# Kernel optimization log

Hardware: AMD Instinct MI355X
Metric: run time of the kernel (lower is better)

Reference implementation:

```python
import jax, jax.numpy as jnp
import numpy as np

EMBED = 1024
HEADS = 16
HEAD_DIM = EMBED // HEADS
BATCH = 2
SUM_LEN = 64
REG_LEN = 2048
BAR = REG_LEN // SUM_LEN  # regular tokens per bar
ROPE_BASE = 10000.0


def _rope_cos_sin(pos, dim):
    inv = 1.0 / (ROPE_BASE ** (jnp.arange(0, dim, 2, dtype=jnp.float32) / dim))
    f = pos[:, None].astype(jnp.float32) * inv[None, :]        # (L, dim/2)
    emb = jnp.concatenate([f, f], axis=-1)                     # (L, dim)
    return jnp.cos(emb)[None, None], jnp.sin(emb)[None, None]  # (1,1,L,dim)


def _rot_half(x):
    d = x.shape[-1] // 2
    return jnp.concatenate([-x[..., d:], x[..., :d]], axis=-1)


def _apply_rope(q, k, cos, sin):
    return q * cos + _rot_half(q) * sin, k * cos + _rot_half(k) * sin


def _linear(x, w, b):
    return x @ w + b  # w: (in, out) == torch W.T


def _split_heads(x):
    b, l, _ = x.shape
    return x.reshape(b, l, HEADS, HEAD_DIM).transpose(0, 2, 1, 3)  # (B,H,L,D)


def _merge_heads(x):
    b, h, l, d = x.shape
    return x.transpose(0, 2, 1, 3).reshape(b, l, h * d)


def _masked_attn(q, k, v, mask):
    # fp32 attention as in the torch autocast-disabled blocks
    qf, kf, vf = q.astype(jnp.float32), k.astype(jnp.float32), v.astype(jnp.float32)
    s = jnp.einsum('bhqd,bhkd->bhqk', qf, kf) / np.sqrt(HEAD_DIM).astype(np.float32)
    s = jnp.where(mask[None, None], s, -jnp.inf)  # every row has >=1 valid key
    p = jax.nn.softmax(s, axis=-1)
    return jnp.einsum('bhqk,bhkd->bhqd', p, vf)


def _build_masks():
    S, R = SUM_LEN, REG_LEN
    bar_of = np.arange(R) // BAR
    ss = np.tril(np.ones((S, S), dtype=bool))
    sr = bar_of[None, :] == np.arange(S)[:, None]
    summarize = np.concatenate([ss, sr], axis=1)              # (S, S+R)
    rs = np.arange(S)[None, :] <= bar_of[:, None]
    rr = (bar_of[None, :] == bar_of[:, None]) & (np.arange(R)[None, :] <= np.arange(R)[:, None])
    updating = np.concatenate([rs, rr], axis=1)               # (R, S+R)
    return jnp.asarray(summarize), jnp.asarray(updating)


def setup_inputs() -> dict:
    key = jax.random.key(0)
    ks = jax.random.split(key, 24)
    inp = {
        'sum_x': jax.random.normal(ks[0], (BATCH, SUM_LEN, EMBED), jnp.float32),
        'reg_x': jax.random.normal(ks[1], (BATCH, REG_LEN, EMBED), jnp.float32),
    }
    sm, um = _build_masks()
    inp['summarize_mask'] = sm
    inp['updating_mask'] = um
    names = ['wq_s', 'wk_s', 'wv_s', 'wo_s', 'wq_r', 'wk_r', 'wv_r', 'wo_r', 'wk2', 'wv2']
    for i, n in enumerate(names):
        inp[n] = jax.random.normal(ks[2 + i], (EMBED, EMBED), jnp.float32) * 0.02
        inp[n.replace('w', 'b', 1)] = jnp.zeros((EMBED,), jnp.float32)
    return inp


def reference(sum_x, reg_x, summarize_mask, updating_mask,
              wq_s, bq_s, wk_s, bk_s, wv_s, bv_s, wo_s, bo_s,
              wq_r, bq_r, wk_r, bk_r, wv_r, bv_r, wo_r, bo_r,
              wk2, bk2, wv2, bv2):
    B, S, E = sum_x.shape
    R = reg_x.shape[1]

    sum_q = _split_heads(_linear(sum_x, wq_s, bq_s))
    sum_k = _split_heads(_linear(sum_x, wk_s, bk_s))
    sum_v = _split_heads(_linear(sum_x, wv_s, bv_s))
    reg_q = _split_heads(_linear(reg_x, wq_r, bq_r))
    reg_k = _split_heads(_linear(reg_x, wk_r, bk_r))
    reg_v = _split_heads(_linear(reg_x, wv_r, bv_r))

    # RoPE: summaries at positions [0,S), regulars at positions [S, S+R)
    cos_s, sin_s = _rope_cos_sin(jnp.arange(S), HEAD_DIM)
    sum_q, sum_k = _apply_rope(sum_q, sum_k, cos_s, sin_s)
    cos_r, sin_r = _rope_cos_sin(jnp.arange(S, S + R), HEAD_DIM)
    reg_q, reg_k = _apply_rope(reg_q, reg_k, cos_r, sin_r)

    # Stage 1: summaries attend over [summary K/V ; regular K/V]
    k1 = jnp.concatenate([sum_k, reg_k], axis=2)
    v1 = jnp.concatenate([sum_v, reg_v], axis=2)
    sum_attn = _merge_heads(_masked_attn(sum_q, k1, v1, summarize_mask))  # (B,S,E)

    # Re-project summary output to K2/V2
    sum_k2 = _split_heads(_linear(sum_attn, wk2, bk2))
    sum_v2 = _split_heads(_linear(sum_attn, wv2, bv2))

    # Stage 2: regulars attend over [summary K2/V2 ; regular K/V]
    k2 = jnp.concatenate([sum_k2, reg_k], axis=2)
    v2 = jnp.concatenate([sum_v2, reg_v], axis=2)
    reg_attn = _merge_heads(_masked_attn(reg_q, k2, v2, updating_mask))   # (B,R,E)

    sum_output = _linear(sum_attn, wo_s, bo_s)
    reg_output = _linear(reg_attn, wo_r, bo_r)
    return sum_output, reg_output
```

## Files before the change

### kernel.cpp

```cpp
#include <hip/hip_runtime.h>
#include <stdint.h>

typedef unsigned short u16;
typedef unsigned int u32;
typedef __attribute__((ext_vector_type(8))) short short8;
typedef __attribute__((ext_vector_type(4))) float f32x4;

#define EMBED 1024
#define HEADS 16
#define HDIM 64
#define NBATCH 2
#define SLEN 64
#define RLEN 2048
#define TOTKV (SLEN + RLEN)

struct B10 { const float* p[10]; };
struct WSrc { const float* p[10]; };

__device__ __forceinline__ float bf2f(u16 u) {
  union { u32 i; float f; } v; v.i = ((u32)u) << 16; return v.f;
}
__device__ __forceinline__ u16 f2bf(float f) {
  union { float f; u32 i; } v; v.f = f;
  return (u16)((v.i + 0x7fffu + ((v.i >> 16) & 1u)) >> 16);
}
__device__ __forceinline__ void up2(u32 u, float& a, float& b) {
  union { u32 i; float f; } x, y;
  x.i = u << 16; y.i = u & 0xffff0000u;
  a = x.f; b = y.f;
}
__device__ __forceinline__ void gload16(const void* g, void* l) {
  __builtin_amdgcn_global_load_lds((const __attribute__((address_space(1))) u32*)g,
                                   (__attribute__((address_space(3))) u32*)l, 16, 0, 0);
}

__global__ __launch_bounds__(256)
void prepass_k(WSrc wsrc, u16* __restrict__ Wt,
               const float* __restrict__ sum_x, u16* __restrict__ sxb,
               const float* __restrict__ reg_x, u16* __restrict__ rxb,
               float* __restrict__ cosT, float* __restrict__ sinT)
{
  __shared__ float tile[64][65];
  int b = blockIdx.x, t = threadIdx.x;
  if (b < 2560) {
    int z = b >> 8, rem = b & 255;
    int n0 = (rem & 15) * 64, k0 = (rem >> 4) * 64;
    const float* src = wsrc.p[z];
    u16* out = Wt + (size_t)z * (EMBED * (size_t)EMBED);
    int r0 = t >> 4, c0 = (t & 15) * 4;
#pragma unroll
    for (int i = 0; i < 4; ++i) {
      int r = i * 16 + r0;
      float4 v = *(const float4*)(src + (size_t)(k0 + r) * EMBED + n0 + c0);
      tile[r][c0] = v.x; tile[r][c0 + 1] = v.y; tile[r][c0 + 2] = v.z; tile[r][c0 + 3] = v.w;
    }
    __syncthreads();
#pragma unroll
    for (int i = 0; i < 4; ++i) {
      int n = i * 16 + r0;
      uint2 o;
      o.x = (u32)f2bf(tile[c0][n]) | ((u32)f2bf(tile[c0 + 1][n]) << 16);
      o.y = (u32)f2bf(tile[c0 + 2][n]) | ((u32)f2bf(tile[c0 + 3][n]) << 16);
      *(uint2*)(out + (size_t)(n0 + n) * EMBED + k0 + c0) = o;
    }
  } else if (b < 6656) {
    int i = ((b - 2560) * 256 + t) * 4;
    if (i < (int)((size_t)NBATCH * RLEN * EMBED)) {
      float4 v = *(const float4*)(reg_x + i);
      uint2 o;
      o.x = (u32)f2bf(v.x) | ((u32)f2bf(v.y) << 16);
      o.y = (u32)f2bf(v.z) | ((u32)f2bf(v.w) << 16);
      *(uint2*)(rxb + i) = o;
    }
  } else if (b < 6784) {
    int i = ((b - 6656) * 256 + t) * 4;
    if (i < (int)((size_t)NBATCH * SLEN * EMBED)) {
      float4 v = *(const float4*)(sum_x + i);
      uint2 o;
      o.x = (u32)f2bf(v.x) | ((u32)f2bf(v.y) << 16);
      o.y = (u32)f2bf(v.z) | ((u32)f2bf(v.w) << 16);
      *(uint2*)(sxb + i) = o;
    }
  } else {
    int idx = (b - 6784) * 256 + t;
    if (idx < TOTKV * 32) {
      int pos = idx >> 5, i = idx & 31;
      float inv = powf(10000.0f, -(float)i / 32.0f);
      float a = (float)pos * inv;
      float s, c;
      sincosf(a, &s, &c);
      cosT[idx] = c; sinT[idx] = s;
    }
  }
}

__device__ __forceinline__ void gemm_core(const u16* __restrict__ A, const u16* __restrict__ Wt,
                                          int rowBase, int colBase, int lane, int w,
                                          u16* As, u16* Bs, f32x4 (&acc)[4][4]) {
  int wr = w >> 1, wc = w & 1;
  int lrow = lane >> 3;
  int lcol = ((lane & 7) ^ lrow) * 8;
  const u16* srcA = A + (size_t)(rowBase + w * 16 + lrow) * EMBED + lcol;
  const u16* srcB = Wt + (size_t)(colBase + w * 16 + lrow) * EMBED + lcol;
  u16* dA = As + w * 1024;
  u16* dB = Bs + w * 1024;
  int l15 = lane & 15, lg = lane >> 4;
  int aoff = l15 * 64 + ((lg ^ (l15 & 7)) * 8);
  const u16* fA = As + wr * 4096 + aoff;
  const u16* fB = Bs + wc * 4096 + aoff;

  for (int k0 = 0; k0 < EMBED; k0 += 64) {
    gload16(srcA + k0, dA);
    gload16(srcA + 8 * EMBED + k0, dA + 512);
    gload16(srcA + 64 * EMBED + k0, dA + 4096);
    gload16(srcA + 72 * EMBED + k0, dA + 4608);
    gload16(srcB + k0, dB);
    gload16(srcB + 8 * EMBED + k0, dB + 512);
    gload16(srcB + 64 * EMBED + k0, dB + 4096);
    gload16(srcB + 72 * EMBED + k0, dB + 4608);
    __syncthreads();
#pragma unroll
    for (int ks = 0; ks < 2; ++ks) {
      const u16* fAk = (const u16*)((uintptr_t)fA ^ (unsigned)(ks << 6));
      const u16* fBk = (const u16*)((uintptr_t)fB ^ (unsigned)(ks << 6));
      short8 af[4], bfv[4];
#pragma unroll
      for (int mi = 0; mi < 4; ++mi) af[mi] = *(const short8*)(fAk + mi * 1024);
#pragma unroll
      for (int ni = 0; ni < 4; ++ni) bfv[ni] = *(const short8*)(fBk + ni * 1024);
#pragma unroll
      for (int mi = 0; mi < 4; ++mi)
#pragma unroll
        for (int ni = 0; ni < 4; ++ni)
          acc[mi][ni] = __builtin_amdgcn_mfma_f32_16x16x32_bf16(af[mi], bfv[ni], acc[mi][ni], 0, 0, 0);
    }
    __syncthreads();
  }
}

__device__ __forceinline__ void gemm_epilogue(f32x4 (&acc)[4][4], int mode, void* outp,
                                              const float* bias, int rowBase, int colBase,
                                              int L, int posoff, int lane, int w,
                                              const float* cosT, const float* sinT) {
  int wr = w >> 1, wc = w & 1;
  int c15 = lane & 15, rgrp = (lane >> 4) * 4;
  if (mode == 2) {
    float* out = (float*)outp;
#pragma unroll
    for (int mi = 0; mi < 4; ++mi)
#pragma unroll
      for (int r = 0; r < 4; ++r) {
        int m = rowBase + wr * 64 + mi * 16 + rgrp + r;
#pragma unroll
        for (int ni = 0; ni < 4; ++ni) {
          int n = colBase + wc * 64 + ni * 16 + c15;
          out[(size_t)m * EMBED + n] = acc[mi][ni][r] + bias[n];
        }
      }
  } else {
    u16* out = (u16*)outp;
    int h = (colBase >> 6) + wc;
    bool dorope = (mode == 0);
#pragma unroll
    for (int mi = 0; mi < 4; ++mi)
#pragma unroll
      for (int r = 0; r < 4; ++r) {
        int m = rowBase + wr * 64 + mi * 16 + rgrp + r;
        int bidx = (m >= L) ? 1 : 0;
        int l = m - bidx * L;
        size_t obase = ((size_t)(bidx * HEADS + h) * L + l) * HDIM;
        if (dorope) {
          int pos = posoff + l;
#pragma unroll
          for (int ni = 0; ni < 2; ++ni) {
            int d = ni * 16 + c15;
            float c = cosT[pos * 32 + d], s = sinT[pos * 32 + d];
            float x0 = acc[mi][ni][r] + bias[h * 64 + d];
            float x2 = acc[mi][ni + 2][r] + bias[h * 64 + d + 32];
            out[obase + d]      = f2bf(x0 * c - x2 * s);
            out[obase + d + 32] = f2bf(x2 * c + x0 * s);
          }
        } else {
#pragma unroll
          for (int ni = 0; ni < 4; ++ni) {
            int d = ni * 16 + c15;
            out[obase + d] = f2bf(acc[mi][ni][r] + bias[h * 64 + d]);
          }
        }
      }
  }
}

__global__ __launch_bounds__(256)
void qkv_gemm_k(const u16* __restrict__ rxb, const u16* __restrict__ sxb,
                const u16* __restrict__ Wt_all, B10 biases,
                u16* Qs, u16* Ks, u16* Vs, u16* Qr, u16* Kr, u16* Vr,
                const float* __restrict__ cosT, const float* __restrict__ sinT)
{
  __shared__ __align__(128) u16 As[8192];
  __shared__ __align__(128) u16 Bs[8192];
  int bx = blockIdx.x, by = blockIdx.y, bz = blockIdx.z;

  bool issum = (by == 0);
  const u16* A = issum ? sxb : rxb;
  int rowBase = issum ? 0 : (by - 1) * 128;
  int L = issum ? SLEN : RLEN;
  int posoff = issum ? 0 : SLEN;
  int widx = issum ? bz : 4 + bz;
  const u16* Wt = Wt_all + (size_t)widx * EMBED * EMBED;
  const float* bias = biases.p[widx];
  u16* out = issum ? (bz == 0 ? Qs : (bz == 1 ? Ks : Vs))
                   : (bz == 0 ? Qr : (bz == 1 ? Kr : Vr));
  int mode = (bz < 2) ? 0 : 1;
  int colBase = bx * 128;
  int lane = threadIdx.x & 63, w = threadIdx.x >> 6;

  f32x4 acc[4][4] = {};
  gemm_core(A, Wt, rowBase, colBase, lane, w, As, Bs, acc);
  gemm_epilogue(acc, mode, out, bias, rowBase, colBase, L, posoff, lane, w, cosT, sinT);
}

__global__ __launch_bounds__(256)
void gemm_k(const u16* __restrict__ A,
            const u16* W0, const u16* W1, const u16* W2,
            const float* b0, const float* b1, const float* b2,
            void* o0, void* o1, void* o2,
            int L, int m0, int m1, int m2, int posoff,
            const float* __restrict__ cosT, const float* __restrict__ sinT)
{
  __shared__ __align__(128) u16 As[8192];
  __shared__ __align__(128) u16 Bs[8192];
  int bx = blockIdx.x, by = blockIdx.y, bz = blockIdx.z;
  const u16* Wt = (bz == 0) ? W0 : ((bz == 1) ? W1 : W2);
  const float* bias = (bz == 0) ? b0 : ((bz == 1) ? b1 : b2);
  void* outp = (bz == 0) ? o0 : ((bz == 1) ? o1 : o2);
  int mode = (bz == 0) ? m0 : ((bz == 1) ? m1 : m2);
  int rowBase = by * 128, colBase = bx * 128;
  int lane = threadIdx.x & 63, w = threadIdx.x >> 6;

  f32x4 acc[4][4] = {};
  gemm_core(A, Wt, rowBase, colBase, lane, w, As, Bs, acc);
  gemm_epilogue(acc, mode, outp, bias, rowBase, colBase, L, posoff, lane, w, cosT, sinT);
}

__global__ __launch_bounds__(256)
void gemm64_k(const u16* __restrict__ A, const u16* __restrict__ Wt,
              const float* __restrict__ bias, float* __restrict__ out)
{
  __shared__ __align__(128) u16 As[8192];
  __shared__ __align__(128) u16 Bs[4096];
  int rowBase = blockIdx.y * 128, colBase = blockIdx.x * 64;
  int lane = threadIdx.x & 63, w = threadIdx.x >> 6;
  int lrow = lane >> 3, lcol = ((lane & 7) ^ lrow) * 8;

  const u16* srcA = A + (size_t)(rowBase + w * 16 + lrow) * EMBED + lcol;
  const u16* srcB = Wt + (size_t)(colBase + w * 16 + lrow) * EMBED + lcol;
  u16* dA = As + w * 1024;
  u16* dB = Bs + w * 1024;
  int l15 = lane & 15, lg = lane >> 4;
  int aoff = l15 * 64 + ((lg ^ (l15 & 7)) * 8);
  const u16* fA = As + w * 2048 + aoff;
  const u16* fB = Bs + aoff;

  f32x4 acc[2][4] = {};
  for (int k0 = 0; k0 < EMBED; k0 += 64) {
    gload16(srcA + k0, dA);
    gload16(srcA + 8 * EMBED + k0, dA + 512);
    gload16(srcA + 64 * EMBED + k0, dA + 4096);
    gload16(srcA + 72 * EMBED + k0, dA + 4608);
    gload16(srcB + k0, dB);
    gload16(srcB + 8 * EMBED + k0, dB + 512);
    __syncthreads();
#pragma unroll
    for (int ks = 0; ks < 2; ++ks) {
      const u16* fAk = (const u16*)((uintptr_t)fA ^ (unsigned)(ks << 6));
      const u16* fBk = (const u16*)((uintptr_t)fB ^ (unsigned)(ks << 6));
      short8 af[2], bfv[4];
#pragma unroll
      for (int mi = 0; mi < 2; ++mi) af[mi] = *(const short8*)(fAk + mi * 1024);
#pragma unroll
      for (int ni = 0; ni < 4; ++ni) bfv[ni] = *(const short8*)(fBk + ni * 1024);
#pragma unroll
      for (int mi = 0; mi < 2; ++mi)
#pragma unroll
        for (int ni = 0; ni < 4; ++ni)
          acc[mi][ni] = __builtin_amdgcn_mfma_f32_16x16x32_bf16(af[mi], bfv[ni], acc[mi][ni], 0, 0, 0);
    }
    __syncthreads();
  }

  int c15 = lane & 15, rgrp = (lane >> 4) * 4;
#pragma unroll
  for (int mi = 0; mi < 2; ++mi)
#pragma unroll
    for (int r = 0; r < 4; ++r) {
      int m = rowBase + w * 32 + mi * 16 + rgrp + r;
#pragma unroll
      for (int ni = 0; ni < 4; ++ni) {
        int n = colBase + ni * 16 + c15;
        out[(size_t)m * EMBED + n] = acc[mi][ni][r] + bias[n];
      }
    }
}

__device__ __forceinline__ void loadq(const u16* qrow, float* qf) {
  const uint4* qp = (const uint4*)qrow;
#pragma unroll
  for (int c = 0; c < 8; ++c) {
    uint4 u = qp[c];
    up2(u.x, qf[c * 8 + 0], qf[c * 8 + 1]);
    up2(u.y, qf[c * 8 + 2], qf[c * 8 + 3]);
    up2(u.z, qf[c * 8 + 4], qf[c * 8 + 5]);
    up2(u.w, qf[c * 8 + 6], qf[c * 8 + 7]);
  }
}
__device__ __forceinline__ float dot64(const float* qf, const u16* krow) {
  const uint4* kp = (const uint4*)krow;
  float s = 0.f;
#pragma unroll
  for (int c = 0; c < 8; ++c) {
    uint4 u = kp[c];
    float a0, a1, a2, a3, a4, a5, a6, a7;
    up2(u.x, a0, a1); up2(u.y, a2, a3); up2(u.z, a4, a5); up2(u.w, a6, a7);
    s += qf[c * 8 + 0] * a0 + qf[c * 8 + 1] * a1 + qf[c * 8 + 2] * a2 + qf[c * 8 + 3] * a3
       + qf[c * 8 + 4] * a4 + qf[c * 8 + 5] * a5 + qf[c * 8 + 6] * a6 + qf[c * 8 + 7] * a7;
  }
  return s;
}

__global__ __launch_bounds__(256)
void attn1_k(const u16* __restrict__ Qs, const u16* __restrict__ Ks,
             const u16* __restrict__ Vs, const u16* __restrict__ Kr,
             const u16* __restrict__ Vr, u16* __restrict__ outA)
{
  int gw = blockIdx.x * 4 + (threadIdx.x >> 6);
  int bh = gw >> 6, qi = gw & 63;
  int b = bh >> 4, h = bh & 15;
  int lane = threadIdx.x & 63;
  const u16* qB = Qs + (size_t)bh * SLEN * HDIM;
  const u16* kS = Ks + (size_t)bh * SLEN * HDIM;
  const u16* vS = Vs + (size_t)bh * SLEN * HDIM;
  const u16* kR = Kr + (size_t)bh * RLEN * HDIM;
  const u16* vR = Vr + (size_t)bh * RLEN * HDIM;

  float qf[64];
  loadq(qB + qi * HDIM, qf);
  bool v1 = (lane <= qi);
  bool v2 = (lane < 32);
  float s1 = v1 ? dot64(qf, kS + lane * HDIM) : 0.f;
  float s2 = v2 ? dot64(qf, kR + (qi * 32 + lane) * HDIM) : 0.f;
  float sc1 = v1 ? s1 * 0.125f : -1e30f;
  float sc2 = v2 ? s2 * 0.125f : -1e30f;
  float mx = fmaxf(sc1, sc2);
#pragma unroll
  for (int off = 32; off; off >>= 1) mx = fmaxf(mx, __shfl_xor(mx, off));
  float e1 = v1 ? __expf(sc1 - mx) : 0.f;
  float e2 = v2 ? __expf(sc2 - mx) : 0.f;
  float sm = e1 + e2;
#pragma unroll
  for (int off = 32; off; off >>= 1) sm += __shfl_xor(sm, off);
  float inv = 1.f / sm;

  float a0 = 0.f, a1 = 0.f, a2 = 0.f, a3 = 0.f;
  const u16* vrow = vR + (size_t)qi * 32 * HDIM + lane;
#pragma unroll
  for (int j = 0; j < 64; j += 4) {
    a0 += __shfl(e1, j + 0) * bf2f(vS[(j + 0) * HDIM + lane]);
    a1 += __shfl(e1, j + 1) * bf2f(vS[(j + 1) * HDIM + lane]);
    a2 += __shfl(e1, j + 2) * bf2f(vS[(j + 2) * HDIM + lane]);
    a3 += __shfl(e1, j + 3) * bf2f(vS[(j + 3) * HDIM + lane]);
  }
#pragma unroll
  for (int j = 0; j < 32; j += 4) {
    a0 += __shfl(e2, j + 0) * bf2f(vrow[(j + 0) * HDIM]);
    a1 += __shfl(e2, j + 1) * bf2f(vrow[(j + 1) * HDIM]);
    a2 += __shfl(e2, j + 2) * bf2f(vrow[(j + 2) * HDIM]);
    a3 += __shfl(e2, j + 3) * bf2f(vrow[(j + 3) * HDIM]);
  }
  float accv = (a0 + a1) + (a2 + a3);
  outA[((size_t)(b * SLEN + qi)) * EMBED + h * HDIM + lane] = f2bf(accv * inv);
}

__global__ __launch_bounds__(256)
void attn2_k(const u16* __restrict__ Qr, const u16* __restrict__ Kr,
             const u16* __restrict__ Vr, const u16* __restrict__ Ks2,
             const u16* __restrict__ Vs2, u16* __restrict__ outA)
{
  __shared__ __align__(16) float Sf[32][104];
  __shared__ __align__(16) u16 Pb[32][104];
  __shared__ __align__(16) u16 Vt[64][104];

  int bar = blockIdx.x, bh = blockIdx.y;
  int b = bh >> 4, h = bh & 15;
  int nS = bar + 1;
  int tid = threadIdx.x, lane = tid & 63, w = tid >> 6;
  int l15 = lane & 15, lg = lane >> 4;

  const u16* qB = Qr + ((size_t)bh * RLEN + bar * 32) * HDIM;
  const u16* kS = Ks2 + (size_t)bh * SLEN * HDIM;
  const u16* kR = Kr + ((size_t)bh * RLEN + bar * 32) * HDIM;
  const u16* vS = Vs2 + (size_t)bh * SLEN * HDIM;
  const u16* vR = Vr + ((size_t)bh * RLEN + bar * 32) * HDIM;

  {
    int keyo = tid >> 3, dg = (tid & 7) * 8;
#pragma unroll
    for (int it = 0; it < 3; ++it) {
      int key = it * 32 + keyo;
      const u16* src = (key < 64) ? (vS + key * 64 + dg) : (vR + (key - 64) * 64 + dg);
      uint4 v = *(const uint4*)src;
#pragma unroll
      for (int wi = 0; wi < 4; ++wi) {
        u32 wv = (wi == 0) ? v.x : (wi == 1) ? v.y : (wi == 2) ? v.z : v.w;
        Vt[dg + 2 * wi][key]     = (u16)(wv & 0xffffu);
        Vt[dg + 2 * wi + 1][key] = (u16)(wv >> 16);
      }
    }
  }

#pragma unroll
  for (int i = 0; i < 3; ++i) {
    int t = w * 3 + i, r = t / 6, c = t % 6;
    const u16* arow = qB + (r * 16 + l15) * 64 + lg * 8;
    const u16* brow = (c < 4) ? (kS + (c * 16 + l15) * 64 + lg * 8)
                              : (kR + ((c - 4) * 16 + l15) * 64 + lg * 8);
    f32x4 acc = {};
    acc = __builtin_amdgcn_mfma_f32_16x16x32_bf16(*(const short8*)arow,
                                                  *(const short8*)brow, acc, 0, 0, 0);
    acc = __builtin_amdgcn_mfma_f32_16x16x32_bf16(*(const short8*)(arow + 32),
                                                  *(const short8*)(brow + 32), acc, 0, 0, 0);
#pragma unroll
    for (int j = 0; j < 4; ++j)
      Sf[r * 16 + lg * 4 + j][c * 16 + l15] = acc[j] * 0.125f;
  }
  __syncthreads();

  {
    int r = w * 8 + (lane >> 3), sub = lane & 7;
    float vals[12];
    float mx = -1e30f;
#pragma unroll
    for (int j = 0; j < 12; ++j) {
      int c = sub + 8 * j;
      bool valid = (c < nS) || (c >= 64 && c < 96 && (c - 64) <= r);
      float v = valid ? Sf[r][c] : -1e30f;
      vals[j] = v;
      mx = fmaxf(mx, v);
    }
#pragma unroll
    for (int off = 1; off < 8; off <<= 1) mx = fmaxf(mx, __shfl_xor(mx, off));
    float sm = 0.f;
#pragma unroll
    for (int j = 0; j < 12; ++j) {
      vals[j] = __expf(vals[j] - mx);
      sm += vals[j];
    }
#pragma unroll
    for (int off = 1; off < 8; off <<= 1) sm += __shfl_xor(sm, off);
    float inv = 1.f / sm;
#pragma unroll
    for (int j = 0; j < 12; ++j) {
      int c = sub + 8 * j;
      Pb[r][c] = f2bf(vals[j] * inv);
    }
  }
  __syncthreads();

#pragma unroll
  for (int i = 0; i < 2; ++i) {
    int t = w * 2 + i, r = t >> 2, dc = t & 3;
    f32x4 acc = {};
#pragma unroll
    for (int ks = 0; ks < 3; ++ks) {
      short8 a = *(const short8*)&Pb[r * 16 + l15][ks * 32 + lg * 8];
      short8 bb = *(const short8*)&Vt[dc * 16 + l15][ks * 32 + lg * 8];
      acc = __builtin_amdgcn_mfma_f32_16x16x32_bf16(a, bb, acc, 0, 0, 0);
    }
    int d = dc * 16 + l15;
#pragma unroll
    for (int j = 0; j < 4; ++j) {
      int qq = r * 16 + lg * 4 + j;
      int tt = bar * 32 + qq;
      outA[((size_t)(b * RLEN + tt)) * EMBED + h * 64 + d] = f2bf(acc[j]);
    }
  }
}

extern "C" void kernel_launch(void* const* d_in, const int* in_sizes, int n_in,
                              void* d_out, int out_size, void* d_ws, size_t ws_size,
                              hipStream_t stream) {
  const float* sum_x = (const float*)d_in[0];
  const float* reg_x = (const float*)d_in[1];
  const float* W[10]; const float* Bv[10];
  for (int i = 0; i < 10; ++i) {
    W[i] = (const float*)d_in[4 + 2 * i];
    Bv[i] = (const float*)d_in[5 + 2 * i];
  }

  char* ws = (char*)d_ws;
  size_t off = 0;
  auto alloc = [&](size_t bytes) -> void* {
    void* p = ws + off;
    off += (bytes + 255) & ~(size_t)255;
    return p;
  };

  const size_t SX = (size_t)NBATCH * SLEN * EMBED;
  const size_t RX = (size_t)NBATCH * RLEN * EMBED;

  float* cosT = (float*)alloc((size_t)TOTKV * 32 * 4);
  float* sinT = (float*)alloc((size_t)TOTKV * 32 * 4);
  u16* sxb = (u16*)alloc(SX * 2);
  u16* rxb = (u16*)alloc(RX * 2);
  u16* Wt  = (u16*)alloc((size_t)10 * EMBED * EMBED * 2);
  u16* Qs = (u16*)alloc(SX * 2);
  u16* Ks = (u16*)alloc(SX * 2);
  u16* Vs = (u16*)alloc(SX * 2);
  u16* Qr = (u16*)alloc(RX * 2);
  u16* Kr = (u16*)alloc(RX * 2);
  u16* Vr = (u16*)alloc(RX * 2);
  u16* sattn = (u16*)alloc(SX * 2);
  u16* Ks2 = (u16*)alloc(SX * 2);
  u16* Vs2 = (u16*)alloc(SX * 2);
  u16* rattn = (u16*)alloc(RX * 2);
  (void)ws_size; (void)in_sizes; (void)n_in; (void)out_size;

  WSrc wsrc;
  for (int i = 0; i < 10; ++i) wsrc.p[i] = W[i];
  B10 biases;
  for (int i = 0; i < 10; ++i) biases.p[i] = Bv[i];

  prepass_k<<<7048, 256, 0, stream>>>(wsrc, Wt, sum_x, sxb, reg_x, rxb, cosT, sinT);

#define WT(i) (Wt + (size_t)(i) * EMBED * EMBED)
  qkv_gemm_k<<<dim3(8, 33, 3), 256, 0, stream>>>(rxb, sxb, Wt, biases,
      Qs, Ks, Vs, Qr, Kr, Vr, cosT, sinT);
  attn1_k<<<512, 256, 0, stream>>>(Qs, Ks, Vs, Kr, Vr, sattn);
  float* outS = (float*)d_out;
  float* outR = outS + SX;
  gemm_k<<<dim3(8, 1, 3), 256, 0, stream>>>(sattn, WT(8), WT(9), WT(3),
      Bv[8], Bv[9], Bv[3], Ks2, Vs2, outS, SLEN, 1, 1, 2, 0, cosT, sinT);
  attn2_k<<<dim3(64, 32), 256, 0, stream>>>(Qr, Kr, Vr, Ks2, Vs2, rattn);
  gemm64_k<<<dim3(16, 32), 256, 0, stream>>>(rattn, WT(7), Bv[7], outR);
#undef WT
}
```

Measured before the change: 147.6 us.

## Use K=32 GEMM tiles in QKV projection and fold summary rows into first row-blocks

Adds a gemm_core32 variant that stages 32-wide K slices, halving LDS use per block, which could allow more resident blocks per CU. The QKV kernel now launches 32 row-blocks instead of 33. The blocks with by==0 compute their regular-token tile and then also the summary-token projection, which removes the separate extra grid row. The cost is twice as many loop iterations and barriers, with no XOR swizzle on the LDS layout, which may cause bank conflicts. It also makes the by==0 blocks do double work, a load-imbalance tail.

```diff
diff --git a/kernel.cpp b/kernel.cpp
--- a/kernel.cpp
+++ b/kernel.cpp
@@ -94,6 +94,41 @@
   }
 }
 
+__device__ __forceinline__ void gemm_core32(const u16* __restrict__ A, const u16* __restrict__ Wt,
+                                            int rowBase, int colBase, int lane, int w,
+                                            u16* As, u16* Bs, f32x4 (&acc)[4][4]) {
+  int wr = w >> 1, wc = w & 1;
+  int lr = lane >> 2, l4 = lane & 3;
+  const u16* srcA0 = A + (size_t)(rowBase + w * 16 + lr) * EMBED + l4 * 8;
+  const u16* srcA1 = srcA0 + 64 * EMBED;
+  const u16* srcB0 = Wt + (size_t)(colBase + w * 16 + lr) * EMBED + l4 * 8;
+  const u16* srcB1 = srcB0 + 64 * EMBED;
+  u16* dstA = As + w * 512;
+  u16* dstB = Bs + w * 512;
+  int aoff = (lane & 15) * 32 + (lane >> 4) * 8;
+  const u16* fA = As + wr * 2048 + aoff;
+  const u16* fB = Bs + wc * 2048 + aoff;
+
+  for (int k0 = 0; k0 < EMBED; k0 += 32) {
+    gload16(srcA0 + k0, dstA);
+    gload16(srcA1 + k0, dstA + 2048);
+    gload16(srcB0 + k0, dstB);
+    gload16(srcB1 + k0, dstB + 2048);
+    __syncthreads();
+    short8 af[4], bfv[4];
+#pragma unroll
+    for (int mi = 0; mi < 4; ++mi) af[mi] = *(const short8*)(fA + mi * 512);
+#pragma unroll
+    for (int ni = 0; ni < 4; ++ni) bfv[ni] = *(const short8*)(fB + ni * 512);
+#pragma unroll
+    for (int mi = 0; mi < 4; ++mi)
+#pragma unroll
+      for (int ni = 0; ni < 4; ++ni)
+        acc[mi][ni] = __builtin_amdgcn_mfma_f32_16x16x32_bf16(af[mi], bfv[ni], acc[mi][ni], 0, 0, 0);
+    __syncthreads();
+  }
+}
+
 __device__ __forceinline__ void gemm_core(const u16* __restrict__ A, const u16* __restrict__ Wt,
                                           int rowBase, int colBase, int lane, int w,
                                           u16* As, u16* Bs, f32x4 (&acc)[4][4]) {
@@ -197,27 +232,27 @@
                 u16* Qs, u16* Ks, u16* Vs, u16* Qr, u16* Kr, u16* Vr,
                 const float* __restrict__ cosT, const float* __restrict__ sinT)
 {
-  __shared__ __align__(128) u16 As[8192];
-  __shared__ __align__(128) u16 Bs[8192];
+  __shared__ __align__(16) u16 As[4096];
+  __shared__ __align__(16) u16 Bs[4096];
   int bx = blockIdx.x, by = blockIdx.y, bz = blockIdx.z;
-
-  bool issum = (by == 0);
-  const u16* A = issum ? sxb : rxb;
-  int rowBase = issum ? 0 : (by - 1) * 128;
-  int L = issum ? SLEN : RLEN;
-  int posoff = issum ? 0 : SLEN;
-  int widx = issum ? bz : 4 + bz;
-  const u16* Wt = Wt_all + (size_t)widx * EMBED * EMBED;
-  const float* bias = biases.p[widx];
-  u16* out = issum ? (bz == 0 ? Qs : (bz == 1 ? Ks : Vs))
-                   : (bz == 0 ? Qr : (bz == 1 ? Kr : Vr));
+  int lane = threadIdx.x & 63, w = threadIdx.x >> 6;
+  int colBase = bx * 128;
   int mode = (bz < 2) ? 0 : 1;
-  int colBase = bx * 128;
-  int lane = threadIdx.x & 63, w = threadIdx.x >> 6;
-
-  f32x4 acc[4][4] = {};
-  gemm_core(A, Wt, rowBase, colBase, lane, w, As, Bs, acc);
-  gemm_epilogue(acc, mode, out, bias, rowBase, colBase, L, posoff, lane, w, cosT, sinT);
+
+  {
+    const u16* Wt = Wt_all + (size_t)(4 + bz) * EMBED * EMBED;
+    u16* out = (bz == 0) ? Qr : (bz == 1 ? Kr : Vr);
+    f32x4 acc[4][4] = {};
+    gemm_core32(rxb, Wt, by * 128, colBase, lane, w, As, Bs, acc);
+    gemm_epilogue(acc, mode, out, biases.p[4 + bz], by * 128, colBase, RLEN, SLEN, lane, w, cosT, sinT);
+  }
+  if (by == 0) {
+    const u16* Wt = Wt_all + (size_t)bz * EMBED * EMBED;
+    u16* out = (bz == 0) ? Qs : (bz == 1 ? Ks : Vs);
+    f32x4 acc[4][4] = {};
+    gemm_core32(sxb, Wt, 0, colBase, lane, w, As, Bs, acc);
+    gemm_epilogue(acc, mode, out, biases.p[bz], 0, colBase, SLEN, 0, lane, w, cosT, sinT);
+  }
 }
 
 __global__ __launch_bounds__(256)
@@ -533,7 +568,7 @@
   prepass_k<<<7048, 256, 0, stream>>>(wsrc, Wt, sum_x, sxb, reg_x, rxb, cosT, sinT);
 
 #define WT(i) (Wt + (size_t)(i) * EMBED * EMBED)
-  qkv_gemm_k<<<dim3(8, 33, 3), 256, 0, stream>>>(rxb, sxb, Wt, biases,
+  qkv_gemm_k<<<dim3(8, 32, 3), 256, 0, stream>>>(rxb, sxb, Wt, biases,
       Qs, Ks, Vs, Qr, Kr, Vr, cosT, sinT);
   attn1_k<<<512, 256, 0, stream>>>(Qs, Ks, Vs, Kr, Vr, sattn);
   float* outS = (float*)d_out;
```

New measurement: 154.0 us. 4.3% more time.
